# Optimization experiments

Measured on AMD Instinct MI355X. Metric: run time of the kernel, lower is better.

Reference implementation:

```python
import jax, jax.numpy as jnp
import numpy as np

B, S, D_MODEL, N_HEADS, D_K, D_V = 2, 2048, 1024, 16, 64, 64


def setup_inputs() -> dict:
    key = jax.random.key(0)
    ks = jax.random.split(key, 11)
    s_in = 1.0 / np.sqrt(D_MODEL)
    s_out = 1.0 / np.sqrt(N_HEADS * D_V)
    return {
        "Q": jax.random.normal(ks[0], (B, S, D_MODEL), jnp.float32),
        "K": jax.random.normal(ks[1], (B, S, D_MODEL), jnp.float32),
        "V": jax.random.normal(ks[2], (B, S, D_MODEL), jnp.float32),
        # per-head projection weights (stacked over heads), Linear-style: y = x @ W + b
        "Wq": jax.random.uniform(ks[3], (N_HEADS, D_MODEL, D_K), jnp.float32, -s_in, s_in),
        "bq": jax.random.uniform(ks[4], (N_HEADS, D_K), jnp.float32, -s_in, s_in),
        "Wk": jax.random.uniform(ks[5], (N_HEADS, D_MODEL, D_K), jnp.float32, -s_in, s_in),
        "bk": jax.random.uniform(ks[6], (N_HEADS, D_K), jnp.float32, -s_in, s_in),
        "Wv": jax.random.uniform(ks[7], (N_HEADS, D_MODEL, D_V), jnp.float32, -s_in, s_in),
        "bv": jax.random.uniform(ks[8], (N_HEADS, D_V), jnp.float32, -s_in, s_in),
        "Wo": jax.random.uniform(ks[9], (N_HEADS * D_V, D_MODEL), jnp.float32, -s_out, s_out),
        "bo": jax.random.uniform(ks[10], (D_MODEL,), jnp.float32, -s_out, s_out),
    }


def reference(Q, K, V, Wq, bq, Wk, bk, Wv, bv, Wo, bo):
    # Per-head projections, batched over heads: [B,H,S,dk/dv]
    QW = jnp.einsum("bsd,hdk->bhsk", Q, Wq) + bq[None, :, None, :]
    KW = jnp.einsum("bsd,hdk->bhsk", K, Wk) + bk[None, :, None, :]
    VW = jnp.einsum("bsd,hdv->bhsv", V, Wv) + bv[None, :, None, :]
    scores = jnp.einsum("bhsk,bhtk->bhst", QW, KW)  # [B,H,S,S]
    # Faithful to torch source: softmax(scores)/d_k**1/2 == softmax(scores)/(2*d_k)
    attn = jax.nn.softmax(scores, axis=-1) * (1.0 / (2.0 * D_K))
    heads = jnp.einsum("bhst,bhtv->bhsv", attn, VW)  # [B,H,S,dv]
    # concat heads along feature dim -> [B,S,H*dv], then output projection
    concat = heads.transpose(0, 2, 1, 3).reshape(B, S, N_HEADS * D_V)
    return concat @ Wo + bo
```

## Files before the change

kernel.cpp:

```cpp
#include <hip/hip_runtime.h>

#define BB 2
#define SS 2048
#define DM 1024
#define HH 16
#define DK 64
#define LOG2E 1.44269504088896340736f

typedef __attribute__((ext_vector_type(8))) short short8;
typedef __attribute__((ext_vector_type(4))) float f32x4;
typedef __attribute__((ext_vector_type(16))) float f32x16;

#define MFMA16(a, b, c) __builtin_amdgcn_mfma_f32_16x16x32_bf16(a, b, c, 0, 0, 0)
#define MFMA32(a, b, c) __builtin_amdgcn_mfma_f32_32x32x16_bf16(a, b, c, 0, 0, 0)

#if __has_builtin(__builtin_amdgcn_exp2f)
#define EXP2(x) __builtin_amdgcn_exp2f(x)
#else
#define EXP2(x) __expf((x) * 0.6931471805599453f)
#endif

#define WAITV(N) asm volatile("s_waitcnt vmcnt(" #N ")" ::: "memory")
#define BAR() __builtin_amdgcn_s_barrier()

static __device__ __forceinline__ unsigned short f2bf(float f) {
    unsigned u = __builtin_bit_cast(unsigned, f);
    u += 0x7fffu + ((u >> 16) & 1u);
    return (unsigned short)(u >> 16);
}
static __device__ __forceinline__ float bf2f(unsigned short u) {
    return __builtin_bit_cast(float, ((unsigned)u) << 16);
}

static __device__ __forceinline__ void gld16(const void* g, void* l) {
    __builtin_amdgcn_global_load_lds(
        (const __attribute__((address_space(1))) unsigned int*)g,
        (__attribute__((address_space(3))) unsigned int*)l, 16, 0, 0);
}

__global__ __launch_bounds__(256) void cvt3_kernel(
    const float* __restrict__ p0, const float* __restrict__ p1,
    const float* __restrict__ p2, unsigned short* __restrict__ o0,
    unsigned short* __restrict__ o1, unsigned short* __restrict__ o2) {
    const int m = blockIdx.y;
    const float* in = m == 0 ? p0 : (m == 1 ? p1 : p2);
    unsigned short* out = m == 0 ? o0 : (m == 1 ? o1 : o2);
    const int i = (blockIdx.x * 256 + threadIdx.x) * 8;
    float4 a = *(const float4*)(in + i);
    float4 b = *(const float4*)(in + i + 4);
    union { unsigned short u[8]; uint4 v; } x;
    x.u[0] = f2bf(a.x); x.u[1] = f2bf(a.y); x.u[2] = f2bf(a.z); x.u[3] = f2bf(a.w);
    x.u[4] = f2bf(b.x); x.u[5] = f2bf(b.y); x.u[6] = f2bf(b.z); x.u[7] = f2bf(b.w);
    *(uint4*)(out + i) = x.v;
}

__global__ __launch_bounds__(256) void wtrans4_kernel(
    const float* __restrict__ Wq, const float* __restrict__ Wk,
    const float* __restrict__ Wv, const float* __restrict__ Wo,
    unsigned short* __restrict__ Wqt, unsigned short* __restrict__ Wkt,
    unsigned short* __restrict__ Wvt, unsigned short* __restrict__ Wot) {
    __shared__ float t[64][65];
    const int which = blockIdx.y;
    const float* in;
    unsigned short* out;
    int r0, c0, C;
    if (which < 3) {
        in = which == 0 ? Wq : (which == 1 ? Wk : Wv);
        out = which == 0 ? Wqt : (which == 1 ? Wkt : Wvt);
        const int h = blockIdx.x >> 4;
        r0 = (blockIdx.x & 15) * 64; c0 = 0; C = DK;
        in += (size_t)h * DM * DK;
        out += (size_t)h * DK * DM;
    } else {
        in = Wo; out = Wot;
        r0 = (blockIdx.x & 15) * 64; c0 = (blockIdx.x >> 4) * 64; C = DM;
    }
    const int lr = threadIdx.x & 63, gg = threadIdx.x >> 6;
    #pragma unroll
    for (int p = 0; p < 16; ++p) {
        const int r = p * 4 + gg;
        t[r][lr] = in[(size_t)(r0 + r) * C + c0 + lr];
    }
    __syncthreads();
    #pragma unroll
    for (int p = 0; p < 16; ++p) {
        const int c = p * 4 + gg;
        out[(size_t)(c0 + c) * DM + r0 + lr] = f2bf(t[lr][c]);
    }
}

#define GSTAGE(Ap, Btp, k0, pp)                                              \
    do {                                                                     \
        _Pragma("unroll")                                                    \
        for (int i = 0; i < 4; ++i) {                                        \
            const int idx = tid + i * 256;                                   \
            const int row = idx >> 3, c8 = (idx & 7) * 8;                    \
            gld16(&Ap[(size_t)(r0 + row) * DM + (k0) + c8], &As[pp][idx * 8]); \
            gld16(&Btp[(size_t)(n0 + row) * DM + (k0) + c8], &Bs[pp][idx * 8]); \
        }                                                                    \
    } while (0)

#define GCOMPUTE(pp)                                                         \
    do {                                                                     \
        _Pragma("unroll")                                                    \
        for (int kc = 0; kc < 2; ++kc) {                                     \
            short8 a[4], b[4];                                               \
            _Pragma("unroll")                                                \
            for (int i = 0; i < 4; ++i) {                                    \
                a[i] = *(const short8*)&As[pp][(wr + i * 16 + lr) * 64 + kc * 32 + lg * 8]; \
                b[i] = *(const short8*)&Bs[pp][(wc + i * 16 + lr) * 64 + kc * 32 + lg * 8]; \
            }                                                                \
            __builtin_amdgcn_s_setprio(1);                                   \
            _Pragma("unroll")                                                \
            for (int mi = 0; mi < 4; ++mi)                                   \
                _Pragma("unroll")                                            \
                for (int ni = 0; ni < 4; ++ni)                               \
                    acc[mi][ni] = MFMA16(a[mi], b[ni], acc[mi][ni]);         \
            __builtin_amdgcn_s_setprio(0);                                   \
        }                                                                    \
    } while (0)

#define GEMM_MAIN(Ap, Btp)                                                   \
    GSTAGE(Ap, Btp, 0, 0);                                                   \
    for (int k = 0; k < 14 * 64; k += 128) {                                 \
        GSTAGE(Ap, Btp, k + 64, 1);                                          \
        WAITV(8); BAR();                                                     \
        GCOMPUTE(0);                                                         \
        BAR();                                                               \
        GSTAGE(Ap, Btp, k + 128, 0);                                         \
        WAITV(8); BAR();                                                     \
        GCOMPUTE(1);                                                         \
        BAR();                                                               \
    }                                                                        \
    GSTAGE(Ap, Btp, 15 * 64, 1);                                             \
    WAITV(8); BAR();                                                         \
    GCOMPUTE(0);                                                             \
    BAR();                                                                   \
    WAITV(0); BAR();                                                         \
    GCOMPUTE(1);

__global__ __launch_bounds__(256) void qkv_gemm_kernel(
    const unsigned short* __restrict__ Qb, const unsigned short* __restrict__ Kb,
    const unsigned short* __restrict__ Vb,
    const unsigned short* __restrict__ Wqt, const unsigned short* __restrict__ Wkt,
    const unsigned short* __restrict__ Wvt,
    const float* __restrict__ bq, const float* __restrict__ bk,
    const float* __restrict__ bv,
    unsigned short* __restrict__ QWp, unsigned short* __restrict__ KWp,
    unsigned short* __restrict__ VWt) {
    __shared__ unsigned short As[2][128 * 64];
    __shared__ unsigned short Bs[2][128 * 64];
    const int z = blockIdx.z;
    const unsigned short* A  = z == 0 ? Qb : (z == 1 ? Kb : Vb);
    const unsigned short* Bt = z == 0 ? Wqt : (z == 1 ? Wkt : Wvt);
    const float* bias = z == 0 ? bq : (z == 1 ? bk : bv);
    const int tid = threadIdx.x;
    const int r0 = blockIdx.x * 128, n0 = blockIdx.y * 128;
    const int w = tid >> 6, lane = tid & 63, lr = lane & 15, lg = lane >> 4;
    const int wr = (w >> 1) * 64, wc = (w & 1) * 64;

    const f32x4 zf = {0.f, 0.f, 0.f, 0.f};
    f32x4 acc[4][4];
    #pragma unroll
    for (int mi = 0; mi < 4; ++mi)
        #pragma unroll
        for (int ni = 0; ni < 4; ++ni) acc[mi][ni] = zf;

    GEMM_MAIN(A, Bt);

    const float scale = (z == 0) ? LOG2E : 1.0f;
    #pragma unroll
    for (int ni = 0; ni < 4; ++ni) {
        const int col = n0 + wc + ni * 16 + lr;
        const float bb = bias[col];
        #pragma unroll
        for (int mi = 0; mi < 4; ++mi) {
            const int rbase = r0 + wr + mi * 16 + lg * 4;
            const f32x4 v = acc[mi][ni];
            if (z == 2) {
                const int b = rbase >> 11, s = rbase & (SS - 1);
                const int h = col >> 6, vv = col & 63;
                union { unsigned short u[4]; unsigned long long q; } x;
                #pragma unroll
                for (int j = 0; j < 4; ++j) x.u[j] = f2bf(v[j] + bb);
                *(unsigned long long*)&VWt[((size_t)(b * HH + h) * 64 + vv) * SS + s] = x.q;
            } else {
                unsigned short* C = z == 0 ? QWp : KWp;
                #pragma unroll
                for (int j = 0; j < 4; ++j)
                    C[(size_t)(rbase + j) * DM + col] = f2bf((v[j] + bb) * scale);
            }
        }
    }
}

__global__ __launch_bounds__(256) void outproj_kernel(
    const unsigned short* __restrict__ A, const unsigned short* __restrict__ Bt,
    const float* __restrict__ bias, float* __restrict__ Cout) {
    __shared__ unsigned short As[2][128 * 64];
    __shared__ unsigned short Bs[2][128 * 64];
    const int tid = threadIdx.x;
    const int r0 = blockIdx.x * 128, n0 = blockIdx.y * 128;
    const int w = tid >> 6, lane = tid & 63, lr = lane & 15, lg = lane >> 4;
    const int wr = (w >> 1) * 64, wc = (w & 1) * 64;

    const f32x4 zf = {0.f, 0.f, 0.f, 0.f};
    f32x4 acc[4][4];
    #pragma unroll
    for (int mi = 0; mi < 4; ++mi)
        #pragma unroll
        for (int ni = 0; ni < 4; ++ni) acc[mi][ni] = zf;

    GEMM_MAIN(A, Bt);

    #pragma unroll
    for (int ni = 0; ni < 4; ++ni) {
        const int col = n0 + wc + ni * 16 + lr;
        const float bb = bias[col];
        #pragma unroll
        for (int mi = 0; mi < 4; ++mi) {
            const int rbase = r0 + wr + mi * 16 + lg * 4;
            const f32x4 v = acc[mi][ni];
            #pragma unroll
            for (int j = 0; j < 4; ++j)
                Cout[(size_t)(rbase + j) * DM + col] = v[j] + bb;
        }
    }
}

#define FRAG(buf, row, col) \
    (*(const short8*)&buf[(row) * 64 + ((col) ^ (((row) & 7) << 3))])

__global__ __launch_bounds__(256, 2) void attn_kernel(
    const unsigned short* __restrict__ QW,
    const unsigned short* __restrict__ KW,
    const unsigned short* __restrict__ VWt,
    unsigned short* __restrict__ Opart,
    float* __restrict__ Lpart) {
    __shared__ unsigned short Ks[2][64 * 64];
    __shared__ unsigned short Vs[2][64 * 64];
    const int tid = threadIdx.x;
    const int w = tid >> 6, lane = tid & 63;
    const int ql = lane & 31, hi = lane >> 5, hi8 = hi * 8;

    const int wgid = blockIdx.x;
    const int kk = wgid >> 3;
    const int bh = (kk >> 5) * 8 + (wgid & 7);
    const int b = bh >> 4, h = bh & 15;
    const int row0 = ((kk & 31) >> 1) * 128;
    const int z = kk & 1;
    const int q = row0 + w * 32 + ql;

    short8 qf[4];
    const unsigned short* Qp = QW + ((size_t)b * SS + q) * DM + h * DK;
    #pragma unroll
    for (int kc = 0; kc < 4; ++kc)
        qf[kc] = *(const short8*)(Qp + kc * 16 + hi8);

    const unsigned short* Kp = KW + (size_t)b * SS * DM + h * DK;
    const unsigned short* Vt = VWt + (size_t)bh * 64 * SS;

    const int sidx0 = tid, sidx1 = tid + 256;
    const int srow0 = sidx0 >> 3, sc0 = ((sidx0 & 7) ^ (srow0 & 7)) * 8;
    const int srow1 = sidx1 >> 3, sc1 = ((sidx1 & 7) ^ (srow1 & 7)) * 8;

#define STAGE(t0, pp)                                                        \
    do {                                                                     \
        gld16(&Kp[(size_t)((t0) + srow0) * DM + sc0], &Ks[pp][sidx0 * 8]);   \
        gld16(&Vt[(size_t)srow0 * SS + (t0) + sc0], &Vs[pp][sidx0 * 8]);     \
        gld16(&Kp[(size_t)((t0) + srow1) * DM + sc1], &Ks[pp][sidx1 * 8]);   \
        gld16(&Vt[(size_t)srow1 * SS + (t0) + sc1], &Vs[pp][sidx1 * 8]);     \
    } while (0)

    const f32x16 z16 = {0.f};
    const short8 ones = {(short)0x3F80, (short)0x3F80, (short)0x3F80, (short)0x3F80,
                         (short)0x3F80, (short)0x3F80, (short)0x3F80, (short)0x3F80};
    f32x16 o0 = z16, o1 = z16, lv = z16;

#define COMPUTE(pp)                                                              \
    do {                                                                         \
        f32x16 s0, s1;                                                           \
        __builtin_amdgcn_s_setprio(1);                                           \
        s0 = MFMA32(FRAG(Ks[pp], ql, hi8), qf[0], z16);                          \
        s1 = MFMA32(FRAG(Ks[pp], 32 + ql, hi8), qf[0], z16);                     \
        _Pragma("unroll")                                                        \
        for (int kc = 1; kc < 4; ++kc) {                                         \
            s0 = MFMA32(FRAG(Ks[pp], ql, kc * 16 + hi8), qf[kc], s0);            \
            s1 = MFMA32(FRAG(Ks[pp], 32 + ql, kc * 16 + hi8), qf[kc], s1);       \
        }                                                                        \
        __builtin_amdgcn_s_setprio(0);                                           \
        _Pragma("unroll")                                                        \
        for (int r = 0; r < 16; ++r) {                                           \
            s0[r] = EXP2(s0[r]);                                                 \
            s1[r] = EXP2(s1[r]);                                                 \
        }                                                                        \
        short8 pa[4];                                                            \
        _Pragma("unroll")                                                        \
        for (int ks = 0; ks < 4; ++ks) {                                         \
            const f32x16 sx = (ks < 2) ? s0 : s1;                                \
            const int b0 = (ks & 1) * 8;                                         \
            unsigned x, x2, y, y2;                                               \
            asm("v_cvt_pk_bf16_f32 %0, %1, %2" : "=v"(x)  : "v"(sx[b0+0]), "v"(sx[b0+1])); \
            asm("v_cvt_pk_bf16_f32 %0, %1, %2" : "=v"(x2) : "v"(sx[b0+2]), "v"(sx[b0+3])); \
            asm("v_cvt_pk_bf16_f32 %0, %1, %2" : "=v"(y)  : "v"(sx[b0+4]), "v"(sx[b0+5])); \
            asm("v_cvt_pk_bf16_f32 %0, %1, %2" : "=v"(y2) : "v"(sx[b0+6]), "v"(sx[b0+7])); \
            asm("v_permlane32_swap_b32 %0, %1" : "+v"(x),  "+v"(y));             \
            asm("v_permlane32_swap_b32 %0, %1" : "+v"(x2), "+v"(y2));            \
            union { unsigned u[4]; short8 s8; } pk;                              \
            pk.u[0] = x; pk.u[1] = x2; pk.u[2] = y; pk.u[3] = y2;                \
            pa[ks] = pk.s8;                                                      \
        }                                                                        \
        __builtin_amdgcn_s_setprio(1);                                          \
        _Pragma("unroll")                                                        \
        for (int ks = 0; ks < 4; ++ks) {                                         \
            o0 = MFMA32(FRAG(Vs[pp], ql, ks * 16 + hi8), pa[ks], o0);            \
            lv = MFMA32(ones, pa[ks], lv);                                       \
            o1 = MFMA32(FRAG(Vs[pp], 32 + ql, ks * 16 + hi8), pa[ks], o1);       \
        }                                                                        \
        __builtin_amdgcn_s_setprio(0);                                          \
    } while (0)

    const int tb = z * (SS / 2);

    STAGE(tb, 0);
    for (int i = 0; i < 14; i += 2) {
        STAGE(tb + (i + 1) * 64, 1);
        WAITV(4); BAR();
        COMPUTE(0);
        BAR();
        STAGE(tb + (i + 2) * 64, 0);
        WAITV(4); BAR();
        COMPUTE(1);
        BAR();
    }
    STAGE(tb + 15 * 64, 1);
    WAITV(4); BAR();
    COMPUTE(0);
    BAR();
    WAITV(0); BAR();
    COMPUTE(1);
#undef STAGE
#undef COMPUTE

    unsigned short* Op = Opart + (((size_t)z * 32 + bh) * SS + q) * 64;
    #pragma unroll
    for (int vt = 0; vt < 2; ++vt) {
        const f32x16 ov = vt ? o1 : o0;
        #pragma unroll
        for (int m2 = 0; m2 < 4; ++m2) {
            union { unsigned short u[4]; unsigned long long q8; } pk;
            #pragma unroll
            for (int c = 0; c < 4; ++c) pk.u[c] = f2bf(ov[m2 * 4 + c]);
            *(unsigned long long*)(Op + vt * 32 + m2 * 8 + hi * 4) = pk.q8;
        }
    }
    if (hi == 0) Lpart[((size_t)z * 32 + bh) * SS + q] = lv[0];
}

__global__ __launch_bounds__(256) void combine_kernel(
    const unsigned short* __restrict__ Opart, const float* __restrict__ Lpart,
    unsigned short* __restrict__ CC) {
    const int idx = blockIdx.x * 256 + threadIdx.x;
    const int v0 = (idx & 7) * 8, q = (idx >> 3) & (SS - 1), bh = idx >> 14;
    const size_t po = ((size_t)bh * SS + q) * 64 + v0;
    const size_t ps = (size_t)32 * SS * 64;
    union { uint4 v; unsigned short u[8]; } ua, ub, uo;
    ua.v = *(const uint4*)(Opart + po);
    ub.v = *(const uint4*)(Opart + ps + po);
    const float l = Lpart[(size_t)bh * SS + q] + Lpart[(size_t)32 * SS + bh * SS + q];
    const float inv = 1.0f / (128.0f * l);
    #pragma unroll
    for (int j = 0; j < 8; ++j)
        uo.u[j] = f2bf((bf2f(ua.u[j]) + bf2f(ub.u[j])) * inv);
    *(uint4*)&CC[((size_t)(bh >> 4) * SS + q) * DM + (bh & 15) * 64 + v0] = uo.v;
}

extern "C" void kernel_launch(void* const* d_in, const int* in_sizes, int n_in,
                              void* d_out, int out_size, void* d_ws, size_t ws_size,
                              hipStream_t stream) {
    const float* Q  = (const float*)d_in[0];
    const float* K  = (const float*)d_in[1];
    const float* V  = (const float*)d_in[2];
    const float* Wq = (const float*)d_in[3];
    const float* bq = (const float*)d_in[4];
    const float* Wk = (const float*)d_in[5];
    const float* bk = (const float*)d_in[6];
    const float* Wv = (const float*)d_in[7];
    const float* bv = (const float*)d_in[8];
    const float* Wo = (const float*)d_in[9];
    const float* bo = (const float*)d_in[10];
    float* out = (float*)d_out;

    unsigned short* ws = (unsigned short*)d_ws;
    const size_t MK = (size_t)BB * SS * DM;
    const size_t WK = (size_t)DM * DM;
    unsigned short* Qb  = ws;
    unsigned short* Kb  = Qb + MK;
    unsigned short* Vb  = Kb + MK;
    unsigned short* Wqt = Vb + MK;
    unsigned short* Wkt = Wqt + WK;
    unsigned short* Wvt = Wkt + WK;
    unsigned short* Wot = Wvt + WK;
    unsigned short* QWp = Wot + WK;
    unsigned short* KWp = QWp + MK;
    unsigned short* VWt = KWp + MK;
    unsigned short* Opart = Kb;
    float*          Lpart = (float*)Wqt;
    unsigned short* CCp   = Qb;

    dim3 blk(256);
    const int M = BB * SS;

    hipLaunchKernelGGL(cvt3_kernel, dim3(MK / 2048, 3), blk, 0, stream,
                       Q, K, V, Qb, Kb, Vb);

    hipLaunchKernelGGL(wtrans4_kernel, dim3(256, 4), blk, 0, stream,
                       Wq, Wk, Wv, Wo, Wqt, Wkt, Wvt, Wot);

    hipLaunchKernelGGL(qkv_gemm_kernel, dim3(M / 128, 8, 3), blk, 0, stream,
                       Qb, Kb, Vb, Wqt, Wkt, Wvt, bq, bk, bv, QWp, KWp, VWt);

    hipLaunchKernelGGL(attn_kernel, dim3(1024), blk, 0, stream,
                       QWp, KWp, VWt, Opart, Lpart);

    hipLaunchKernelGGL(combine_kernel, dim3((32 * SS * 8) / 256), blk, 0, stream,
                       Opart, Lpart, CCp);

    hipLaunchKernelGGL(outproj_kernel, dim3(M / 128, 8), blk, 0, stream,
                       CCp, Wot, bo, out);
}
```

Measured before the change: 134.8 us.

## Drop split-K attention and combine kernel; normalize inside attention epilogue

Attention no longer splits the key sequence into two halves with partial outputs merged by a separate combine kernel. Each workgroup now iterates over all 32 key tiles, normalizes by the row sum in the epilogue and writes bf16 directly into the concatenated head layout. This removes one kernel launch plus the partial-output write and read traffic, but halves the grid to 512 workgroups, which may leave CUs underused. Exp and pack are also interleaved per 32-row half so PV MFMAs on the first half can overlap the exponentials of the second.

```diff
diff --git a/kernel.cpp b/kernel.cpp
--- a/kernel.cpp
+++ b/kernel.cpp
@@ -235,8 +235,7 @@
     const unsigned short* __restrict__ QW,
     const unsigned short* __restrict__ KW,
     const unsigned short* __restrict__ VWt,
-    unsigned short* __restrict__ Opart,
-    float* __restrict__ Lpart) {
+    unsigned short* __restrict__ CC) {
     __shared__ unsigned short Ks[2][64 * 64];
     __shared__ unsigned short Vs[2][64 * 64];
     const int tid = threadIdx.x;
@@ -245,10 +244,9 @@
 
     const int wgid = blockIdx.x;
     const int kk = wgid >> 3;
-    const int bh = (kk >> 5) * 8 + (wgid & 7);
+    const int bh = (kk >> 4) * 8 + (wgid & 7);
     const int b = bh >> 4, h = bh & 15;
-    const int row0 = ((kk & 31) >> 1) * 128;
-    const int z = kk & 1;
+    const int row0 = (kk & 15) * 128;
     const int q = row0 + w * 32 + ql;
 
     short8 qf[4];
@@ -276,6 +274,27 @@
     const short8 ones = {(short)0x3F80, (short)0x3F80, (short)0x3F80, (short)0x3F80,
                          (short)0x3F80, (short)0x3F80, (short)0x3F80, (short)0x3F80};
     f32x16 o0 = z16, o1 = z16, lv = z16;
+
+#define PACK2(sx, pa0, pa1)                                                      \
+    do {                                                                         \
+        unsigned x, x2, y, y2, u, u2, v, v2;                                     \
+        asm("v_cvt_pk_bf16_f32 %0, %1, %2" : "=v"(x)  : "v"(sx[0]), "v"(sx[1])); \
+        asm("v_cvt_pk_bf16_f32 %0, %1, %2" : "=v"(x2) : "v"(sx[2]), "v"(sx[3])); \
+        asm("v_cvt_pk_bf16_f32 %0, %1, %2" : "=v"(y)  : "v"(sx[4]), "v"(sx[5])); \
+        asm("v_cvt_pk_bf16_f32 %0, %1, %2" : "=v"(y2) : "v"(sx[6]), "v"(sx[7])); \
+        asm("v_cvt_pk_bf16_f32 %0, %1, %2" : "=v"(u)  : "v"(sx[8]), "v"(sx[9])); \
+        asm("v_cvt_pk_bf16_f32 %0, %1, %2" : "=v"(u2) : "v"(sx[10]), "v"(sx[11])); \
+        asm("v_cvt_pk_bf16_f32 %0, %1, %2" : "=v"(v)  : "v"(sx[12]), "v"(sx[13])); \
+        asm("v_cvt_pk_bf16_f32 %0, %1, %2" : "=v"(v2) : "v"(sx[14]), "v"(sx[15])); \
+        asm("v_permlane32_swap_b32 %0, %1" : "+v"(x),  "+v"(y));                 \
+        asm("v_permlane32_swap_b32 %0, %1" : "+v"(x2), "+v"(y2));                \
+        asm("v_permlane32_swap_b32 %0, %1" : "+v"(u),  "+v"(v));                 \
+        asm("v_permlane32_swap_b32 %0, %1" : "+v"(u2), "+v"(v2));                \
+        union { unsigned uu[4]; short8 s8; } k0, k1;                             \
+        k0.uu[0] = x; k0.uu[1] = x2; k0.uu[2] = y; k0.uu[3] = y2;                \
+        k1.uu[0] = u; k1.uu[1] = u2; k1.uu[2] = v; k1.uu[3] = v2;                \
+        pa0 = k0.s8; pa1 = k1.s8;                                                \
+    } while (0)
 
 #define COMPUTE(pp)                                                              \
     do {                                                                         \
@@ -290,50 +309,42 @@
         }                                                                        \
         __builtin_amdgcn_s_setprio(0);                                           \
         _Pragma("unroll")                                                        \
-        for (int r = 0; r < 16; ++r) {                                           \
-            s0[r] = EXP2(s0[r]);                                                 \
-            s1[r] = EXP2(s1[r]);                                                 \
-        }                                                                        \
-        short8 pa[4];                                                            \
+        for (int r = 0; r < 16; ++r) s0[r] = EXP2(s0[r]);                        \
+        short8 pa0, pa1, pa2, pa3;                                               \
+        PACK2(s0, pa0, pa1);                                                     \
+        __builtin_amdgcn_s_setprio(1);                                           \
+        o0 = MFMA32(FRAG(Vs[pp], ql, hi8), pa0, o0);                             \
+        lv = MFMA32(ones, pa0, lv);                                              \
+        o1 = MFMA32(FRAG(Vs[pp], 32 + ql, hi8), pa0, o1);                        \
+        o0 = MFMA32(FRAG(Vs[pp], ql, 16 + hi8), pa1, o0);                        \
+        lv = MFMA32(ones, pa1, lv);                                              \
+        o1 = MFMA32(FRAG(Vs[pp], 32 + ql, 16 + hi8), pa1, o1);                   \
+        __builtin_amdgcn_s_setprio(0);                                           \
         _Pragma("unroll")                                                        \
-        for (int ks = 0; ks < 4; ++ks) {                                         \
-            const f32x16 sx = (ks < 2) ? s0 : s1;                                \
-            const int b0 = (ks & 1) * 8;                                         \
-            unsigned x, x2, y, y2;                                               \
-            asm("v_cvt_pk_bf16_f32 %0, %1, %2" : "=v"(x)  : "v"(sx[b0+0]), "v"(sx[b0+1])); \
-            asm("v_cvt_pk_bf16_f32 %0, %1, %2" : "=v"(x2) : "v"(sx[b0+2]), "v"(sx[b0+3])); \
-            asm("v_cvt_pk_bf16_f32 %0, %1, %2" : "=v"(y)  : "v"(sx[b0+4]), "v"(sx[b0+5])); \
-            asm("v_cvt_pk_bf16_f32 %0, %1, %2" : "=v"(y2) : "v"(sx[b0+6]), "v"(sx[b0+7])); \
-            asm("v_permlane32_swap_b32 %0, %1" : "+v"(x),  "+v"(y));             \
-            asm("v_permlane32_swap_b32 %0, %1" : "+v"(x2), "+v"(y2));            \
-            union { unsigned u[4]; short8 s8; } pk;                              \
-            pk.u[0] = x; pk.u[1] = x2; pk.u[2] = y; pk.u[3] = y2;                \
-            pa[ks] = pk.s8;                                                      \
-        }                                                                        \
-        __builtin_amdgcn_s_setprio(1);                                          \
-        _Pragma("unroll")                                                        \
-        for (int ks = 0; ks < 4; ++ks) {                                         \
-            o0 = MFMA32(FRAG(Vs[pp], ql, ks * 16 + hi8), pa[ks], o0);            \
-            lv = MFMA32(ones, pa[ks], lv);                                       \
-            o1 = MFMA32(FRAG(Vs[pp], 32 + ql, ks * 16 + hi8), pa[ks], o1);       \
-        }                                                                        \
-        __builtin_amdgcn_s_setprio(0);                                          \
+        for (int r = 0; r < 16; ++r) s1[r] = EXP2(s1[r]);                        \
+        PACK2(s1, pa2, pa3);                                                     \
+        __builtin_amdgcn_s_setprio(1);                                           \
+        o0 = MFMA32(FRAG(Vs[pp], ql, 32 + hi8), pa2, o0);                        \
+        lv = MFMA32(ones, pa2, lv);                                              \
+        o1 = MFMA32(FRAG(Vs[pp], 32 + ql, 32 + hi8), pa2, o1);                   \
+        o0 = MFMA32(FRAG(Vs[pp], ql, 48 + hi8), pa3, o0);                        \
+        lv = MFMA32(ones, pa3, lv);                                              \
+        o1 = MFMA32(FRAG(Vs[pp], 32 + ql, 48 + hi8), pa3, o1);                   \
+        __builtin_amdgcn_s_setprio(0);                                           \
     } while (0)
 
-    const int tb = z * (SS / 2);
-
-    STAGE(tb, 0);
-    for (int i = 0; i < 14; i += 2) {
-        STAGE(tb + (i + 1) * 64, 1);
+    STAGE(0, 0);
+    for (int i = 0; i < 30; i += 2) {
+        STAGE((i + 1) * 64, 1);
         WAITV(4); BAR();
         COMPUTE(0);
         BAR();
-        STAGE(tb + (i + 2) * 64, 0);
+        STAGE((i + 2) * 64, 0);
         WAITV(4); BAR();
         COMPUTE(1);
         BAR();
     }
-    STAGE(tb + 15 * 64, 1);
+    STAGE(31 * 64, 1);
     WAITV(4); BAR();
     COMPUTE(0);
     BAR();
@@ -342,7 +353,8 @@
 #undef STAGE
 #undef COMPUTE
 
-    unsigned short* Op = Opart + (((size_t)z * 32 + bh) * SS + q) * 64;
+    const float inv = 1.0f / (lv[0] * 128.0f);
+    unsigned short* cp = CC + ((size_t)b * SS + q) * DM + h * DK;
     #pragma unroll
     for (int vt = 0; vt < 2; ++vt) {
         const f32x16 ov = vt ? o1 : o0;
@@ -350,29 +362,10 @@
         for (int m2 = 0; m2 < 4; ++m2) {
             union { unsigned short u[4]; unsigned long long q8; } pk;
             #pragma unroll
-            for (int c = 0; c < 4; ++c) pk.u[c] = f2bf(ov[m2 * 4 + c]);
-            *(unsigned long long*)(Op + vt * 32 + m2 * 8 + hi * 4) = pk.q8;
+            for (int c = 0; c < 4; ++c) pk.u[c] = f2bf(ov[m2 * 4 + c] * inv);
+            *(unsigned long long*)(cp + vt * 32 + m2 * 8 + hi * 4) = pk.q8;
         }
     }
-    if (hi == 0) Lpart[((size_t)z * 32 + bh) * SS + q] = lv[0];
-}
-
-__global__ __launch_bounds__(256) void combine_kernel(
-    const unsigned short* __restrict__ Opart, const float* __restrict__ Lpart,
-    unsigned short* __restrict__ CC) {
-    const int idx = blockIdx.x * 256 + threadIdx.x;
-    const int v0 = (idx & 7) * 8, q = (idx >> 3) & (SS - 1), bh = idx >> 14;
-    const size_t po = ((size_t)bh * SS + q) * 64 + v0;
-    const size_t ps = (size_t)32 * SS * 64;
-    union { uint4 v; unsigned short u[8]; } ua, ub, uo;
-    ua.v = *(const uint4*)(Opart + po);
-    ub.v = *(const uint4*)(Opart + ps + po);
-    const float l = Lpart[(size_t)bh * SS + q] + Lpart[(size_t)32 * SS + bh * SS + q];
-    const float inv = 1.0f / (128.0f * l);
-    #pragma unroll
-    for (int j = 0; j < 8; ++j)
-        uo.u[j] = f2bf((bf2f(ua.u[j]) + bf2f(ub.u[j])) * inv);
-    *(uint4*)&CC[((size_t)(bh >> 4) * SS + q) * DM + (bh & 15) * 64 + v0] = uo.v;
 }
 
 extern "C" void kernel_launch(void* const* d_in, const int* in_sizes, int n_in,
@@ -404,9 +397,7 @@
     unsigned short* QWp = Wot + WK;
     unsigned short* KWp = QWp + MK;
     unsigned short* VWt = KWp + MK;
-    unsigned short* Opart = Kb;
-    float*          Lpart = (float*)Wqt;
-    unsigned short* CCp   = Qb;
+    unsigned short* CCp = Qb;
 
     dim3 blk(256);
     const int M = BB * SS;
@@ -420,11 +411,8 @@
     hipLaunchKernelGGL(qkv_gemm_kernel, dim3(M / 128, 8, 3), blk, 0, stream,
                        Qb, Kb, Vb, Wqt, Wkt, Wvt, bq, bk, bv, QWp, KWp, VWt);
 
-    hipLaunchKernelGGL(attn_kernel, dim3(1024), blk, 0, stream,
-                       QWp, KWp, VWt, Opart, Lpart);
-
-    hipLaunchKernelGGL(combine_kernel, dim3((32 * SS * 8) / 256), blk, 0, stream,
-                       Opart, Lpart, CCp);
+    hipLaunchKernelGGL(attn_kernel, dim3(512), blk, 0, stream,
+                       QWp, KWp, VWt, CCp);
 
     hipLaunchKernelGGL(outproj_kernel, dim3(M / 128, 8), blk, 0, stream,
                        CCp, Wot, bo, out);
```

Measured after the change: 127.1 us. -5.7%, faster.
